# Performance work log

Measured on AMD Instinct MI355X. Metric: run time of the kernel, lower is better.

The kernel has to match this reference:

```python
import jax, jax.numpy as jnp
import numpy as np

NUM_HEADS = 8
ATTN_DIM = 512
DIM_HEAD = ATTN_DIM // NUM_HEADS
SCALE = DIM_HEAD ** -0.5
GN_EPS = 1e-5


def setup_inputs() -> dict:
    key = jax.random.key(0)
    k1, k2, k3 = jax.random.split(key, 3)
    B, H, W, C_IN, C_OUT = 8, 32, 32, 256, 256
    x = jax.random.normal(k1, (B, H, W, C_IN), dtype=jnp.float32)
    w_qkv = jax.random.normal(k2, (C_IN, 3 * ATTN_DIM), dtype=jnp.float32) * (C_IN ** -0.5)
    w_out = jax.random.normal(k3, (ATTN_DIM, C_OUT), dtype=jnp.float32) * (ATTN_DIM ** -0.5)
    b_out = jnp.zeros((C_OUT,), dtype=jnp.float32)
    gamma = jnp.ones((C_OUT,), dtype=jnp.float32)
    beta = jnp.zeros((C_OUT,), dtype=jnp.float32)
    return {"x": x, "w_qkv": w_qkv, "w_out": w_out, "b_out": b_out, "gamma": gamma, "beta": beta}


def reference(x, w_qkv, w_out, b_out, gamma, beta):
    B, H, W, _ = x.shape
    N = H * W
    # 1x1 conv QKV projection (no bias)
    qkv = jnp.einsum('bhwc,cd->bhwd', x, w_qkv)
    q, k, v = jnp.split(qkv, 3, axis=-1)
    # NHWC -> (B, heads, dim_head, HW), matching tf transpose+reshape
    def to_heads(t):
        return t.transpose(0, 3, 1, 2).reshape(B, NUM_HEADS, DIM_HEAD, N)
    q = to_heads(q) * SCALE
    k = to_heads(k)
    v = to_heads(v)
    # sim = q^T k over dim_head: (B, heads, N_q, N_k)
    sim = jnp.einsum('bhcn,bhcm->bhnm', q, k)
    attn = jax.nn.softmax(sim, axis=-1)  # includes the max-subtraction of the original
    # out = attn @ v^T: (B, heads, N, dim_head)
    out = jnp.einsum('bhnm,bhcm->bhnc', attn, v)
    # faithful tf.reshape((B,-1,H,W)) then NCHW->NHWC transpose
    out = out.reshape(B, -1, H, W).transpose(0, 2, 3, 1)  # (B, H, W, attn_dim)
    # output 1x1 conv (with bias) + GroupNorm(groups=1): normalize over (H, W, C) per sample
    y = jnp.einsum('bhwc,cd->bhwd', out, w_out) + b_out
    mean = jnp.mean(y, axis=(1, 2, 3), keepdims=True)
    var = jnp.var(y, axis=(1, 2, 3), keepdims=True)
    y = (y - mean) * jax.lax.rsqrt(var + GN_EPS)
    return y * gamma + beta
```

## Files before the change

### kernel.cpp

```cpp
#include <hip/hip_runtime.h>
#include <math.h>

#define NPOS   1024
#define CIN    256
#define DQKV   1536
#define ATTND  512
#define HEADS  8
#define DH     64
#define COUT   256
#define NBATCH 8
#define SCALE  0.125f
#define GN_EPS 1e-5f

typedef __attribute__((ext_vector_type(8))) __bf16 bf16x8;
typedef __attribute__((ext_vector_type(4))) __bf16 bf16x4;
typedef __attribute__((ext_vector_type(4))) float floatx4;
typedef __attribute__((ext_vector_type(8))) unsigned short ushort8;

#if __has_builtin(__builtin_amdgcn_exp2f)
#define EXP2(x) __builtin_amdgcn_exp2f(x)
#else
#define EXP2(x) exp2f(x)
#endif

#define GLOAD16(G, L) __builtin_amdgcn_global_load_lds( \
    (const __attribute__((address_space(1))) void*)(G), \
    (__attribute__((address_space(3))) void*)(L), 16, 0, 0)

#define OFF_XB   (0ull)
#define OFF_WT   (4ull*1048576)
#define OFF_WOT  (4ull*1048576 + 786432ull)
#define OFF_QB   (5ull*1048576)
#define OFF_KB   (13ull*1048576)
#define OFF_VT   (29ull*1048576)
#define OFF_O2TT (45ull*1048576)
#define OFF_ST   (53ull*1048576)

__device__ inline ushort8 cvt_bf8(float4 a, float4 b) {
    bf16x8 o;
    o[0] = (__bf16)a.x; o[1] = (__bf16)a.y; o[2] = (__bf16)a.z; o[3] = (__bf16)a.w;
    o[4] = (__bf16)b.x; o[5] = (__bf16)b.y; o[6] = (__bf16)b.z; o[7] = (__bf16)b.w;
    return *(ushort8*)&o;
}

__global__ __launch_bounds__(256) void prep(
    const float* __restrict__ x,
    const float* __restrict__ w_qkv, const float* __restrict__ w_out,
    unsigned short* __restrict__ xb,
    unsigned short* __restrict__ wT, unsigned short* __restrict__ woT,
    float* __restrict__ stats)
{
    const int bid = blockIdx.x;
    const int t = threadIdx.x;
    __shared__ unsigned short tile[64][68];

    if (bid == 0) stats[t] = 0.0f;

    if (bid >= 128) {
        const size_t base = (size_t)(bid - 128) * 8192 + (size_t)t * 8;
        #pragma unroll
        for (int i = 0; i < 4; ++i) {
            const size_t off = base + (size_t)i * 2048;
            const float4 u = *(const float4*)&x[off];
            const float4 v = *(const float4*)&x[off + 4];
            *(ushort8*)&xb[off] = cvt_bf8(u, v);
        }
        return;
    }

    if (bid < 96) {
        const int n0 = (bid >> 2) * 64, k0 = (bid & 3) * 64;
        #pragma unroll
        for (int p = 0; p < 4; ++p) {
            const int row = p * 16 + (t >> 4);
            const int c = (t & 15) * 4;
            float4 a = *(const float4*)&w_qkv[(size_t)(k0 + row) * DQKV + n0 + c];
            float sv[4] = {a.x, a.y, a.z, a.w};
            #pragma unroll
            for (int j = 0; j < 4; ++j) {
                const float sc = (n0 + c + j) < 512 ? (SCALE * 1.44269504088896f) : 1.0f;
                __bf16 hb = (__bf16)(sv[j] * sc);
                tile[row][c + j] = *(unsigned short*)&hb;
            }
        }
        __syncthreads();
        const int nn = t >> 2;
        const int kc = (t & 3) * 16;
        unsigned short tmp[16];
        #pragma unroll
        for (int j = 0; j < 16; ++j) tmp[j] = tile[kc + j][nn];
        *(ushort8*)&wT[(size_t)(n0 + nn) * 256 + k0 + kc]     = *(ushort8*)&tmp[0];
        *(ushort8*)&wT[(size_t)(n0 + nn) * 256 + k0 + kc + 8] = *(ushort8*)&tmp[8];
        return;
    }

    const int idx = bid - 96;
    const int d0 = (idx & 3) * 64, k0 = (idx >> 2) * 64;
    #pragma unroll
    for (int p = 0; p < 4; ++p) {
        const int row = p * 16 + (t >> 4);
        const int c = (t & 15) * 4;
        float4 a = *(const float4*)&w_out[(size_t)(k0 + row) * COUT + d0 + c];
        float sv[4] = {a.x, a.y, a.z, a.w};
        #pragma unroll
        for (int j = 0; j < 4; ++j) {
            __bf16 hb = (__bf16)sv[j];
            tile[row][c + j] = *(unsigned short*)&hb;
        }
    }
    __syncthreads();
    {
        const int nn = t >> 2;
        const int kc = (t & 3) * 16;
        unsigned short tmp[16];
        #pragma unroll
        for (int j = 0; j < 16; ++j) tmp[j] = tile[kc + j][nn];
        *(ushort8*)&woT[(size_t)(d0 + nn) * 512 + k0 + kc]     = *(ushort8*)&tmp[0];
        *(ushort8*)&woT[(size_t)(d0 + nn) * 512 + k0 + kc + 8] = *(ushort8*)&tmp[8];
    }
}

__global__ __launch_bounds__(256) void qkv_gemm_mfma(
    const unsigned short* __restrict__ xb, const __bf16* __restrict__ wT,
    __bf16* __restrict__ qb, __bf16* __restrict__ kb, __bf16* __restrict__ vT)
{
    const int bid = blockIdx.x;
    const int xcd = bid & 7, local = bid >> 3;
    const int m0 = (xcd * 8 + (local & 7)) * 128;
    const int n0 = (local >> 3) * 128;

    const int t = threadIdx.x;
    const int w = t >> 6, lane = t & 63;
    const int col = lane & 15, qd = lane >> 4;
    const int wm = w >> 1, wn = w & 1;

    __shared__ __align__(16) unsigned short As[2][128][32];
    __shared__ __align__(16) unsigned short Bs[2][128][32];

    floatx4 zero4 = {0.f, 0.f, 0.f, 0.f};
    floatx4 acc[4][4];
    #pragma unroll
    for (int i = 0; i < 4; ++i)
        #pragma unroll
        for (int j = 0; j < 4; ++j) acc[i][j] = zero4;

    const int arow = lane >> 2;
    const int soff = (((lane & 3) ^ ((lane >> 3) & 3)) << 4);
    const char* xsrc = (const char*)xb + (size_t)(m0 + w * 16 + arow) * 512 + soff;
    const char* wsrc = (const char*)wT + (size_t)(n0 + w * 16 + arow) * 512 + soff;

#define QSTAGE(B, KK) do {                                            \
    GLOAD16(xsrc + (KK) * 64,             &As[B][w * 16][0]);         \
    GLOAD16(xsrc + 32768 + (KK) * 64,     &As[B][64 + w * 16][0]);    \
    GLOAD16(wsrc + (KK) * 64,             &Bs[B][w * 16][0]);         \
    GLOAD16(wsrc + 32768 + (KK) * 64,     &Bs[B][64 + w * 16][0]);    \
} while (0)

    QSTAGE(0, 0);
    __syncthreads();

    const int rsw = ((col >> 1) & 3);
    const int fro = ((qd ^ rsw) << 4);

    int cur = 0;
    for (int kk = 0; kk < 8; ++kk) {
        if (kk < 7) QSTAGE(cur ^ 1, kk + 1);

        bf16x8 wf[4];
        #pragma unroll
        for (int ct = 0; ct < 4; ++ct)
            wf[ct] = *(const bf16x8*)((const char*)&Bs[cur][wn * 64 + ct * 16 + col][0] + fro);
        #pragma unroll
        for (int st = 0; st < 4; ++st) {
            bf16x8 xf = *(const bf16x8*)((const char*)&As[cur][wm * 64 + st * 16 + col][0] + fro);
            #pragma unroll
            for (int ct = 0; ct < 4; ++ct)
                acc[ct][st] = __builtin_amdgcn_mfma_f32_16x16x32_bf16(wf[ct], xf, acc[ct][st], 0, 0, 0);
        }
        __syncthreads();
        cur ^= 1;
    }
#undef QSTAGE

    #pragma unroll
    for (int ct = 0; ct < 4; ++ct) {
        const int cbase = n0 + wn * 64 + ct * 16;
        const int sect = cbase >> 9;
        const int hh = (cbase >> 6) & 7;
        const int dd = (cbase & 63) + qd * 4;
        if (sect < 2) {
            __bf16* base = (sect == 0) ? qb : kb;
            #pragma unroll
            for (int st = 0; st < 4; ++st) {
                const int m = m0 + wm * 64 + st * 16 + col;
                const int b_ = m >> 10, n = m & 1023;
                bf16x4 o;
                #pragma unroll
                for (int r = 0; r < 4; ++r) o[r] = (__bf16)acc[ct][st][r];
                *(bf16x4*)&base[(((size_t)b_ * HEADS + hh) * NPOS + n) * DH + dd] = o;
            }
        } else {
            #pragma unroll
            for (int st = 0; st < 4; ++st) {
                const int m = m0 + wm * 64 + st * 16 + col;
                const int b_ = m >> 10, n = m & 1023;
                const size_t rowbase = ((size_t)(b_ * HEADS + hh) * DH + dd) * NPOS + n;
                #pragma unroll
                for (int r = 0; r < 4; ++r)
                    vT[rowbase + (size_t)r * NPOS] = (__bf16)acc[ct][st][r];
            }
        }
    }
}

__global__ __launch_bounds__(256, 2) void attn_mfma(
    const __bf16* __restrict__ qg, const __bf16* __restrict__ kg,
    const __bf16* __restrict__ vTg, __bf16* __restrict__ o2tT)
{
    const int bid = blockIdx.x;
    const int rid = (bid & 7) * 64 + (bid >> 3);
    const int qblk = rid & 7, h = (rid >> 3) & 7, b = rid >> 6;
    const int bh = b * HEADS + h;
    const int t = threadIdx.x;
    const int w = t >> 6, lane = t & 63;
    const int col = lane & 15;
    const int qd = lane >> 4;

    __shared__ __align__(16) unsigned short Kbuf[2][64][64];
    __shared__ __align__(16) unsigned short Vbuf[2][64][64];
    __shared__ __align__(16) unsigned short ps[4][32][68];

    bf16x8 qf0[2], qf1[2];
    #pragma unroll
    for (int s = 0; s < 2; ++s) {
        const __bf16* qptr = qg + ((size_t)bh * NPOS + qblk * 128 + s * 64 + w * 16 + col) * DH;
        qf0[s] = *(const bf16x8*)(qptr + qd * 8);
        qf1[s] = *(const bf16x8*)(qptr + 32 + qd * 8);
    }

    const char* kByte = (const char*)kg  + (size_t)bh * NPOS * DH * 2;
    const char* vByte = (const char*)vTg + (size_t)bh * DH * NPOS * 2;
    const int rsub = lane >> 3;
    const int csw  = ((lane & 7) * 16) ^ (rsub << 4);
    const char* ksrc0 = kByte + (size_t)(w * 8 + rsub) * 128  + csw;
    const char* vsrc0 = vByte + (size_t)(w * 8 + rsub) * 2048 + csw;

#define STAGE(B, KT) do {                                                    \
    const char* ks_ = ksrc0 + (size_t)(KT) * 8192;                           \
    const char* vs_ = vsrc0 + (size_t)(KT) * 128;                            \
    GLOAD16(ks_,         &Kbuf[B][0][0] + w * 512);                          \
    GLOAD16(ks_ + 4096,  &Kbuf[B][0][0] + 2048 + w * 512);                   \
    GLOAD16(vs_,         &Vbuf[B][0][0] + w * 512);                          \
    GLOAD16(vs_ + 65536, &Vbuf[B][0][0] + 2048 + w * 512);                   \
} while (0)

    floatx4 zero4 = {0.f, 0.f, 0.f, 0.f};
    floatx4 accO[2][4];
    #pragma unroll
    for (int s = 0; s < 2; ++s)
        #pragma unroll
        for (int i = 0; i < 4; ++i) accO[s][i] = zero4;
    floatx4 accL[2] = {zero4, zero4};
    bf16x8 ones8;
    #pragma unroll
    for (int j = 0; j < 8; ++j) ones8[j] = (__bf16)1.0f;

    const int swzc = (col & 7) << 4;
    const int offF0 = (qd * 16) ^ swzc;
    const int offF1 = (64 + qd * 16) ^ swzc;

    STAGE(0, 0);
    __syncthreads();

    int cur = 0;
    for (int kt = 0; kt < 16; ++kt) {
        if (kt < 15) STAGE(cur ^ 1, kt + 1);

        floatx4 accS[2][4];
        #pragma unroll
        for (int mt = 0; mt < 4; ++mt) {
            const char* krow = (const char*)&Kbuf[cur][mt * 16 + col][0];
            bf16x8 kf0 = *(const bf16x8*)(krow + offF0);
            bf16x8 kf1 = *(const bf16x8*)(krow + offF1);
            #pragma unroll
            for (int s = 0; s < 2; ++s) {
                accS[s][mt] = __builtin_amdgcn_mfma_f32_16x16x32_bf16(kf0, qf0[s], zero4, 0, 0, 0);
                accS[s][mt] = __builtin_amdgcn_mfma_f32_16x16x32_bf16(kf1, qf1[s], accS[s][mt], 0, 0, 0);
            }
        }

        #pragma unroll
        for (int s = 0; s < 2; ++s)
            #pragma unroll
            for (int mt = 0; mt < 4; ++mt) {
                bf16x4 pv;
                #pragma unroll
                for (int r = 0; r < 4; ++r) pv[r] = (__bf16)EXP2(accS[s][mt][r]);
                *(bf16x4*)&ps[w][s * 16 + col][mt * 16 + qd * 4] = pv;
            }

        bf16x8 pf0[2], pf1[2];
        #pragma unroll
        for (int s = 0; s < 2; ++s) {
            pf0[s] = *(const bf16x8*)&ps[w][s * 16 + col][qd * 8];
            pf1[s] = *(const bf16x8*)&ps[w][s * 16 + col][32 + qd * 8];
            accL[s] = __builtin_amdgcn_mfma_f32_16x16x32_bf16(ones8, pf0[s], accL[s], 0, 0, 0);
            accL[s] = __builtin_amdgcn_mfma_f32_16x16x32_bf16(ones8, pf1[s], accL[s], 0, 0, 0);
        }

        #pragma unroll
        for (int ct = 0; ct < 4; ++ct) {
            const char* vrow = (const char*)&Vbuf[cur][ct * 16 + col][0];
            bf16x8 vf0 = *(const bf16x8*)(vrow + offF0);
            bf16x8 vf1 = *(const bf16x8*)(vrow + offF1);
            #pragma unroll
            for (int s = 0; s < 2; ++s) {
                accO[s][ct] = __builtin_amdgcn_mfma_f32_16x16x32_bf16(vf0, pf0[s], accO[s][ct], 0, 0, 0);
                accO[s][ct] = __builtin_amdgcn_mfma_f32_16x16x32_bf16(vf1, pf1[s], accO[s][ct], 0, 0, 0);
            }
        }
        __syncthreads();
        cur ^= 1;
    }
#undef STAGE

    float inv_l[2];
    #pragma unroll
    for (int s = 0; s < 2; ++s) inv_l[s] = 1.0f / accL[s][0];

    unsigned short (*obuf)[8][68] = (unsigned short (*)[8][68])ps;
    __syncthreads();
    #pragma unroll
    for (int s = 0; s < 2; ++s)
        #pragma unroll
        for (int ct = 0; ct < 4; ++ct) {
            bf16x4 o;
            #pragma unroll
            for (int r = 0; r < 4; ++r) o[r] = (__bf16)(accO[s][ct][r] * inv_l[s]);
            *(bf16x4*)&obuf[col][s * 4 + w][ct * 16 + qd * 4] = o;
        }
    __syncthreads();
    const int chbase = h * 64 + qblk * 8;
    #pragma unroll
    for (int i = 0; i < 4; ++i) {
        const int p = i * 256 + t;
        const int pc = p >> 6, cc = p & 63;
        bf16x8 o;
        #pragma unroll
        for (int j = 0; j < 8; ++j) {
            unsigned short u = obuf[pc][j][cc];
            o[j] = *(__bf16*)&u;
        }
        *(bf16x8*)&o2tT[((size_t)b * NPOS + p) * ATTND + chbase] = o;
    }
}

__global__ __launch_bounds__(256) void out_mfma(
    const __bf16* __restrict__ a, const __bf16* __restrict__ woT,
    const float* __restrict__ b_out, float* __restrict__ y,
    float* __restrict__ stats)
{
    const int bid = blockIdx.x;
    const int xcd = bid & 7, local = bid >> 3;
    const int m0 = (xcd * 16 + (local & 15)) * 64;
    const int d0 = (local >> 4) * 64;
    const int b = xcd;

    const int t = threadIdx.x;
    const int w = t >> 6, lane = t & 63;
    const int col = lane & 15, qd = lane >> 4;
    const int wm = w >> 1, wn = w & 1;

    __shared__ __align__(16) unsigned short As[64][72];
    __shared__ __align__(16) unsigned short Bs[64][72];
    __shared__ float reds[4], redq[4];

    floatx4 zero4 = {0.f, 0.f, 0.f, 0.f};
    floatx4 acc[2][2];
    #pragma unroll
    for (int i = 0; i < 2; ++i)
        #pragma unroll
        for (int j = 0; j < 2; ++j) acc[i][j] = zero4;

    const int lrow = t >> 2, lc = (t & 3) * 16;

    for (int k0 = 0; k0 < ATTND; k0 += 64) {
        __syncthreads();
        *(ushort8*)&As[lrow][lc]     = *(const ushort8*)&a[(size_t)(m0 + lrow) * ATTND + k0 + lc];
        *(ushort8*)&As[lrow][lc + 8] = *(const ushort8*)&a[(size_t)(m0 + lrow) * ATTND + k0 + lc + 8];
        *(ushort8*)&Bs[lrow][lc]     = *(const ushort8*)&woT[(size_t)(d0 + lrow) * ATTND + k0 + lc];
        *(ushort8*)&Bs[lrow][lc + 8] = *(const ushort8*)&woT[(size_t)(d0 + lrow) * ATTND + k0 + lc + 8];
        __syncthreads();
        bf16x8 af0[2], af1[2];
        #pragma unroll
        for (int mt = 0; mt < 2; ++mt) {
            af0[mt] = *(const bf16x8*)&As[wm * 32 + mt * 16 + col][qd * 8];
            af1[mt] = *(const bf16x8*)&As[wm * 32 + mt * 16 + col][32 + qd * 8];
        }
        #pragma unroll
        for (int nt = 0; nt < 2; ++nt) {
            bf16x8 bf0 = *(const bf16x8*)&Bs[wn * 32 + nt * 16 + col][qd * 8];
            bf16x8 bf1 = *(const bf16x8*)&Bs[wn * 32 + nt * 16 + col][32 + qd * 8];
            #pragma unroll
            for (int mt = 0; mt < 2; ++mt) {
                acc[mt][nt] = __builtin_amdgcn_mfma_f32_16x16x32_bf16(af0[mt], bf0, acc[mt][nt], 0, 0, 0);
                acc[mt][nt] = __builtin_amdgcn_mfma_f32_16x16x32_bf16(af1[mt], bf1, acc[mt][nt], 0, 0, 0);
            }
        }
    }

    float bias_n[2];
    #pragma unroll
    for (int nt = 0; nt < 2; ++nt) bias_n[nt] = b_out[d0 + wn * 32 + nt * 16 + col];

    float bsum = 0.0f, bsq = 0.0f;
    #pragma unroll
    for (int mt = 0; mt < 2; ++mt) {
        #pragma unroll
        for (int r = 0; r < 4; ++r) {
            const int m = m0 + wm * 32 + mt * 16 + qd * 4 + r;
            const int p = m & 1023;
            #pragma unroll
            for (int nt = 0; nt < 2; ++nt) {
                const int d = d0 + wn * 32 + nt * 16 + col;
                const float v = acc[mt][nt][r] + bias_n[nt];
                y[((size_t)b * NPOS + p) * COUT + d] = v;
                bsum += v;
                bsq  += v * v;
            }
        }
    }
    #pragma unroll
    for (int off = 1; off < 64; off <<= 1) {
        bsum += __shfl_xor(bsum, off);
        bsq  += __shfl_xor(bsq, off);
    }
    if (lane == 0) { reds[w] = bsum; redq[w] = bsq; }
    __syncthreads();
    if (t == 0) {
        atomicAdd(&stats[b * 16],       reds[0] + reds[1] + reds[2] + reds[3]);
        atomicAdd(&stats[128 + b * 16], redq[0] + redq[1] + redq[2] + redq[3]);
    }
}

__global__ __launch_bounds__(256) void gn_finalize(
    float* __restrict__ y, const float* __restrict__ stats,
    const float* __restrict__ gamma, const float* __restrict__ beta)
{
    const int idx = blockIdx.x * 256 + threadIdx.x;
    const int e = idx * 4;
    const int b_ = e >> 18;
    const int d = e & (COUT - 1);
    const float invn = 1.0f / (float)(NPOS * COUT);
    const float mean = stats[b_ * 16] * invn;
    const float var  = stats[128 + b_ * 16] * invn - mean * mean;
    const float rsig = rsqrtf(var + GN_EPS);
    float4 vv = *(float4*)&y[e];
    const float4 g  = *(const float4*)&gamma[d];
    const float4 bt = *(const float4*)&beta[d];
    vv.x = (vv.x - mean) * rsig * g.x + bt.x;
    vv.y = (vv.y - mean) * rsig * g.y + bt.y;
    vv.z = (vv.z - mean) * rsig * g.z + bt.z;
    vv.w = (vv.w - mean) * rsig * g.w + bt.w;
    *(float4*)&y[e] = vv;
}

extern "C" void kernel_launch(void* const* d_in, const int* in_sizes, int n_in,
                              void* d_out, int out_size, void* d_ws, size_t ws_size,
                              hipStream_t stream)
{
    const float* x     = (const float*)d_in[0];
    const float* w_qkv = (const float*)d_in[1];
    const float* w_out = (const float*)d_in[2];
    const float* b_out = (const float*)d_in[3];
    const float* gamma = (const float*)d_in[4];
    const float* beta  = (const float*)d_in[5];
    float* out = (float*)d_out;
    char* ws = (char*)d_ws;

    unsigned short* xb  = (unsigned short*)(ws + OFF_XB);
    unsigned short* wT  = (unsigned short*)(ws + OFF_WT);
    unsigned short* woT = (unsigned short*)(ws + OFF_WOT);
    __bf16* qb  = (__bf16*)(ws + OFF_QB);
    __bf16* kb  = (__bf16*)(ws + OFF_KB);
    __bf16* vT  = (__bf16*)(ws + OFF_VT);
    __bf16* o2tT = (__bf16*)(ws + OFF_O2TT);
    float* stats = (float*)(ws + OFF_ST);

    prep         <<<dim3(384),  256, 0, stream>>>(x, w_qkv, w_out, xb, wT, woT, stats);
    qkv_gemm_mfma<<<dim3(768),  256, 0, stream>>>(xb, (const __bf16*)wT, qb, kb, vT);
    attn_mfma    <<<dim3(512),  256, 0, stream>>>(qb, kb, vT, o2tT);
    out_mfma     <<<dim3(512),  256, 0, stream>>>(o2tT, (const __bf16*)woT, b_out, out, stats);
    gn_finalize  <<<dim3(2048), 256, 0, stream>>>(out, stats, gamma, beta);
}
```

Before: 124.6 us.

## Fuse all five stages into one cooperative persistent kernel with grid syncs

Merges the prep, QKV GEMM, attention, output GEMM and GroupNorm finalize kernels into a single cooperative kernel of 512 blocks that separates the stages with grid.sync(). The aim is to remove four kernel launch boundaries and the gaps between them. The QKV GEMM's 768 tiles become a grid-stride loop, and all stages share one shared-memory buffer. The cost is a fixed grid size, occupancy limited to two blocks per CU, and grid-wide barrier overhead, with the old multi-kernel path kept as a fallback if the cooperative launch fails.

```diff
diff --git a/kernel.cpp b/kernel.cpp
--- a/kernel.cpp
+++ b/kernel.cpp
@@ -1,5 +1,8 @@
 #include <hip/hip_runtime.h>
+#include <hip/hip_cooperative_groups.h>
 #include <math.h>
+
+namespace cg = cooperative_groups;
 
 #define NPOS   1024
 #define CIN    256
@@ -41,6 +44,414 @@
     o[0] = (__bf16)a.x; o[1] = (__bf16)a.y; o[2] = (__bf16)a.z; o[3] = (__bf16)a.w;
     o[4] = (__bf16)b.x; o[5] = (__bf16)b.y; o[6] = (__bf16)b.z; o[7] = (__bf16)b.w;
     return *(ushort8*)&o;
+}
+
+__global__ __launch_bounds__(256, 2) void mega(
+    const float* __restrict__ x, const float* __restrict__ w_qkv,
+    const float* __restrict__ w_out, const float* __restrict__ b_out,
+    const float* __restrict__ gamma, const float* __restrict__ beta,
+    float* __restrict__ y,
+    unsigned short* __restrict__ xb, unsigned short* __restrict__ wT,
+    unsigned short* __restrict__ woT,
+    __bf16* __restrict__ qb, __bf16* __restrict__ kb, __bf16* __restrict__ vT,
+    __bf16* __restrict__ o2tT, float* __restrict__ stats)
+{
+    cg::grid_group grid = cg::this_grid();
+    const int bid = blockIdx.x;
+    const int t = threadIdx.x;
+    __shared__ __align__(16) unsigned char SM[50176];
+
+    if (bid < 384) {
+        unsigned short (*tile)[68] = (unsigned short (*)[68])SM;
+        if (bid == 0) stats[t] = 0.0f;
+        if (bid >= 128) {
+            const size_t base = (size_t)(bid - 128) * 8192 + (size_t)t * 8;
+            #pragma unroll
+            for (int i = 0; i < 4; ++i) {
+                const size_t off = base + (size_t)i * 2048;
+                const float4 u = *(const float4*)&x[off];
+                const float4 v = *(const float4*)&x[off + 4];
+                *(ushort8*)&xb[off] = cvt_bf8(u, v);
+            }
+        } else if (bid < 96) {
+            const int n0 = (bid >> 2) * 64, k0 = (bid & 3) * 64;
+            #pragma unroll
+            for (int p = 0; p < 4; ++p) {
+                const int row = p * 16 + (t >> 4);
+                const int c = (t & 15) * 4;
+                float4 a = *(const float4*)&w_qkv[(size_t)(k0 + row) * DQKV + n0 + c];
+                float sv[4] = {a.x, a.y, a.z, a.w};
+                #pragma unroll
+                for (int j = 0; j < 4; ++j) {
+                    const float sc = (n0 + c + j) < 512 ? (SCALE * 1.44269504088896f) : 1.0f;
+                    __bf16 hb = (__bf16)(sv[j] * sc);
+                    tile[row][c + j] = *(unsigned short*)&hb;
+                }
+            }
+            __syncthreads();
+            const int nn = t >> 2;
+            const int kc = (t & 3) * 16;
+            unsigned short tmp[16];
+            #pragma unroll
+            for (int j = 0; j < 16; ++j) tmp[j] = tile[kc + j][nn];
+            *(ushort8*)&wT[(size_t)(n0 + nn) * 256 + k0 + kc]     = *(ushort8*)&tmp[0];
+            *(ushort8*)&wT[(size_t)(n0 + nn) * 256 + k0 + kc + 8] = *(ushort8*)&tmp[8];
+        } else {
+            const int idx = bid - 96;
+            const int d0 = (idx & 3) * 64, k0 = (idx >> 2) * 64;
+            #pragma unroll
+            for (int p = 0; p < 4; ++p) {
+                const int row = p * 16 + (t >> 4);
+                const int c = (t & 15) * 4;
+                float4 a = *(const float4*)&w_out[(size_t)(k0 + row) * COUT + d0 + c];
+                float sv[4] = {a.x, a.y, a.z, a.w};
+                #pragma unroll
+                for (int j = 0; j < 4; ++j) {
+                    __bf16 hb = (__bf16)sv[j];
+                    tile[row][c + j] = *(unsigned short*)&hb;
+                }
+            }
+            __syncthreads();
+            const int nn = t >> 2;
+            const int kc = (t & 3) * 16;
+            unsigned short tmp[16];
+            #pragma unroll
+            for (int j = 0; j < 16; ++j) tmp[j] = tile[kc + j][nn];
+            *(ushort8*)&woT[(size_t)(d0 + nn) * 512 + k0 + kc]     = *(ushort8*)&tmp[0];
+            *(ushort8*)&woT[(size_t)(d0 + nn) * 512 + k0 + kc + 8] = *(ushort8*)&tmp[8];
+        }
+    }
+    grid.sync();
+
+    {
+        unsigned short (*As)[128][32] = (unsigned short (*)[128][32])SM;
+        unsigned short (*Bs)[128][32] = (unsigned short (*)[128][32])(SM + 16384);
+        const int w = t >> 6, lane = t & 63;
+        const int col = lane & 15, qd = lane >> 4;
+        const int wm = w >> 1, wn = w & 1;
+        const int arow = lane >> 2;
+        const int soff = (((lane & 3) ^ ((lane >> 3) & 3)) << 4);
+        const int rsw = ((col >> 1) & 3);
+        const int fro = ((qd ^ rsw) << 4);
+        floatx4 zero4 = {0.f, 0.f, 0.f, 0.f};
+
+#define QSTAGE(B, KK) do {                                            \
+    GLOAD16(xsrc + (KK) * 64,             &As[B][w * 16][0]);         \
+    GLOAD16(xsrc + 32768 + (KK) * 64,     &As[B][64 + w * 16][0]);    \
+    GLOAD16(wsrc + (KK) * 64,             &Bs[B][w * 16][0]);         \
+    GLOAD16(wsrc + 32768 + (KK) * 64,     &Bs[B][64 + w * 16][0]);    \
+} while (0)
+
+        for (int tid = bid; tid < 768; tid += 512) {
+            const int xcd = tid & 7, local = tid >> 3;
+            const int m0 = (xcd * 8 + (local & 7)) * 128;
+            const int n0 = (local >> 3) * 128;
+
+            floatx4 acc[4][4];
+            #pragma unroll
+            for (int i = 0; i < 4; ++i)
+                #pragma unroll
+                for (int j = 0; j < 4; ++j) acc[i][j] = zero4;
+
+            const char* xsrc = (const char*)xb + (size_t)(m0 + w * 16 + arow) * 512 + soff;
+            const char* wsrc = (const char*)wT + (size_t)(n0 + w * 16 + arow) * 512 + soff;
+
+            __syncthreads();
+            QSTAGE(0, 0);
+            __syncthreads();
+
+            int cur = 0;
+            for (int kk = 0; kk < 8; ++kk) {
+                if (kk < 7) QSTAGE(cur ^ 1, kk + 1);
+                bf16x8 wf[4];
+                #pragma unroll
+                for (int ct = 0; ct < 4; ++ct)
+                    wf[ct] = *(const bf16x8*)((const char*)&Bs[cur][wn * 64 + ct * 16 + col][0] + fro);
+                #pragma unroll
+                for (int st = 0; st < 4; ++st) {
+                    bf16x8 xf = *(const bf16x8*)((const char*)&As[cur][wm * 64 + st * 16 + col][0] + fro);
+                    #pragma unroll
+                    for (int ct = 0; ct < 4; ++ct)
+                        acc[ct][st] = __builtin_amdgcn_mfma_f32_16x16x32_bf16(wf[ct], xf, acc[ct][st], 0, 0, 0);
+                }
+                __syncthreads();
+                cur ^= 1;
+            }
+
+            #pragma unroll
+            for (int ct = 0; ct < 4; ++ct) {
+                const int cbase = n0 + wn * 64 + ct * 16;
+                const int sect = cbase >> 9;
+                const int hh = (cbase >> 6) & 7;
+                const int dd = (cbase & 63) + qd * 4;
+                if (sect < 2) {
+                    __bf16* base = (sect == 0) ? qb : kb;
+                    #pragma unroll
+                    for (int st = 0; st < 4; ++st) {
+                        const int m = m0 + wm * 64 + st * 16 + col;
+                        const int b_ = m >> 10, n = m & 1023;
+                        bf16x4 o;
+                        #pragma unroll
+                        for (int r = 0; r < 4; ++r) o[r] = (__bf16)acc[ct][st][r];
+                        *(bf16x4*)&base[(((size_t)b_ * HEADS + hh) * NPOS + n) * DH + dd] = o;
+                    }
+                } else {
+                    #pragma unroll
+                    for (int st = 0; st < 4; ++st) {
+                        const int m = m0 + wm * 64 + st * 16 + col;
+                        const int b_ = m >> 10, n = m & 1023;
+                        const size_t rowbase = ((size_t)(b_ * HEADS + hh) * DH + dd) * NPOS + n;
+                        #pragma unroll
+                        for (int r = 0; r < 4; ++r)
+                            vT[rowbase + (size_t)r * NPOS] = (__bf16)acc[ct][st][r];
+                    }
+                }
+            }
+        }
+#undef QSTAGE
+    }
+    grid.sync();
+
+    {
+        unsigned short (*Kbuf)[64][64] = (unsigned short (*)[64][64])SM;
+        unsigned short (*Vbuf)[64][64] = (unsigned short (*)[64][64])(SM + 16384);
+        unsigned short (*ps)[32][68]   = (unsigned short (*)[32][68])(SM + 32768);
+
+        const int rid = (bid & 7) * 64 + (bid >> 3);
+        const int qblk = rid & 7, h = (rid >> 3) & 7, b = rid >> 6;
+        const int bh = b * HEADS + h;
+        const int w = t >> 6, lane = t & 63;
+        const int col = lane & 15;
+        const int qd = lane >> 4;
+
+        bf16x8 qf0[2], qf1[2];
+        #pragma unroll
+        for (int s = 0; s < 2; ++s) {
+            const __bf16* qptr = qb + ((size_t)bh * NPOS + qblk * 128 + s * 64 + w * 16 + col) * DH;
+            qf0[s] = *(const bf16x8*)(qptr + qd * 8);
+            qf1[s] = *(const bf16x8*)(qptr + 32 + qd * 8);
+        }
+
+        const char* kByte = (const char*)kb + (size_t)bh * NPOS * DH * 2;
+        const char* vByte = (const char*)vT + (size_t)bh * DH * NPOS * 2;
+        const int rsub = lane >> 3;
+        const int csw  = ((lane & 7) * 16) ^ (rsub << 4);
+        const char* ksrc0 = kByte + (size_t)(w * 8 + rsub) * 128  + csw;
+        const char* vsrc0 = vByte + (size_t)(w * 8 + rsub) * 2048 + csw;
+
+#define STAGE(B, KT) do {                                                    \
+    const char* ks_ = ksrc0 + (size_t)(KT) * 8192;                           \
+    const char* vs_ = vsrc0 + (size_t)(KT) * 128;                            \
+    GLOAD16(ks_,         &Kbuf[B][0][0] + w * 512);                          \
+    GLOAD16(ks_ + 4096,  &Kbuf[B][0][0] + 2048 + w * 512);                   \
+    GLOAD16(vs_,         &Vbuf[B][0][0] + w * 512);                          \
+    GLOAD16(vs_ + 65536, &Vbuf[B][0][0] + 2048 + w * 512);                   \
+} while (0)
+
+        floatx4 zero4 = {0.f, 0.f, 0.f, 0.f};
+        floatx4 accO[2][4];
+        #pragma unroll
+        for (int s = 0; s < 2; ++s)
+            #pragma unroll
+            for (int i = 0; i < 4; ++i) accO[s][i] = zero4;
+        floatx4 accL[2] = {zero4, zero4};
+        bf16x8 ones8;
+        #pragma unroll
+        for (int j = 0; j < 8; ++j) ones8[j] = (__bf16)1.0f;
+
+        const int swzc = (col & 7) << 4;
+        const int offF0 = (qd * 16) ^ swzc;
+        const int offF1 = (64 + qd * 16) ^ swzc;
+
+        STAGE(0, 0);
+        __syncthreads();
+
+        int cur = 0;
+        for (int kt = 0; kt < 16; ++kt) {
+            if (kt < 15) STAGE(cur ^ 1, kt + 1);
+
+            floatx4 accS[2][4];
+            #pragma unroll
+            for (int mt = 0; mt < 4; ++mt) {
+                const char* krow = (const char*)&Kbuf[cur][mt * 16 + col][0];
+                bf16x8 kf0 = *(const bf16x8*)(krow + offF0);
+                bf16x8 kf1 = *(const bf16x8*)(krow + offF1);
+                #pragma unroll
+                for (int s = 0; s < 2; ++s) {
+                    accS[s][mt] = __builtin_amdgcn_mfma_f32_16x16x32_bf16(kf0, qf0[s], zero4, 0, 0, 0);
+                    accS[s][mt] = __builtin_amdgcn_mfma_f32_16x16x32_bf16(kf1, qf1[s], accS[s][mt], 0, 0, 0);
+                }
+            }
+
+            #pragma unroll
+            for (int s = 0; s < 2; ++s)
+                #pragma unroll
+                for (int mt = 0; mt < 4; ++mt) {
+                    bf16x4 pv;
+                    #pragma unroll
+                    for (int r = 0; r < 4; ++r) pv[r] = (__bf16)EXP2(accS[s][mt][r]);
+                    *(bf16x4*)&ps[w][s * 16 + col][mt * 16 + qd * 4] = pv;
+                }
+
+            bf16x8 pf0[2], pf1[2];
+            #pragma unroll
+            for (int s = 0; s < 2; ++s) {
+                pf0[s] = *(const bf16x8*)&ps[w][s * 16 + col][qd * 8];
+                pf1[s] = *(const bf16x8*)&ps[w][s * 16 + col][32 + qd * 8];
+                accL[s] = __builtin_amdgcn_mfma_f32_16x16x32_bf16(ones8, pf0[s], accL[s], 0, 0, 0);
+                accL[s] = __builtin_amdgcn_mfma_f32_16x16x32_bf16(ones8, pf1[s], accL[s], 0, 0, 0);
+            }
+
+            #pragma unroll
+            for (int ct = 0; ct < 4; ++ct) {
+                const char* vrow = (const char*)&Vbuf[cur][ct * 16 + col][0];
+                bf16x8 vf0 = *(const bf16x8*)(vrow + offF0);
+                bf16x8 vf1 = *(const bf16x8*)(vrow + offF1);
+                #pragma unroll
+                for (int s = 0; s < 2; ++s) {
+                    accO[s][ct] = __builtin_amdgcn_mfma_f32_16x16x32_bf16(vf0, pf0[s], accO[s][ct], 0, 0, 0);
+                    accO[s][ct] = __builtin_amdgcn_mfma_f32_16x16x32_bf16(vf1, pf1[s], accO[s][ct], 0, 0, 0);
+                }
+            }
+            __syncthreads();
+            cur ^= 1;
+        }
+#undef STAGE
+
+        float inv_l[2];
+        #pragma unroll
+        for (int s = 0; s < 2; ++s) inv_l[s] = 1.0f / accL[s][0];
+
+        unsigned short (*obuf)[8][68] = (unsigned short (*)[8][68])ps;
+        __syncthreads();
+        #pragma unroll
+        for (int s = 0; s < 2; ++s)
+            #pragma unroll
+            for (int ct = 0; ct < 4; ++ct) {
+                bf16x4 o;
+                #pragma unroll
+                for (int r = 0; r < 4; ++r) o[r] = (__bf16)(accO[s][ct][r] * inv_l[s]);
+                *(bf16x4*)&obuf[col][s * 4 + w][ct * 16 + qd * 4] = o;
+            }
+        __syncthreads();
+        const int chbase = h * 64 + qblk * 8;
+        #pragma unroll
+        for (int i = 0; i < 4; ++i) {
+            const int p = i * 256 + t;
+            const int pc = p >> 6, cc = p & 63;
+            bf16x8 o;
+            #pragma unroll
+            for (int j = 0; j < 8; ++j) {
+                unsigned short u = obuf[pc][j][cc];
+                o[j] = *(__bf16*)&u;
+            }
+            *(bf16x8*)&o2tT[((size_t)b * NPOS + p) * ATTND + chbase] = o;
+        }
+    }
+    grid.sync();
+
+    {
+        unsigned short (*oAs)[72] = (unsigned short (*)[72])SM;
+        unsigned short (*oBs)[72] = (unsigned short (*)[72])(SM + 16384);
+        float* reds = (float*)(SM + 32768);
+        float* redq = reds + 4;
+
+        const int xcd = bid & 7, local = bid >> 3;
+        const int m0 = (xcd * 16 + (local & 15)) * 64;
+        const int d0 = (local >> 4) * 64;
+        const int b = xcd;
+
+        const int w = t >> 6, lane = t & 63;
+        const int col = lane & 15, qd = lane >> 4;
+        const int wm = w >> 1, wn = w & 1;
+
+        floatx4 zero4 = {0.f, 0.f, 0.f, 0.f};
+        floatx4 acc[2][2];
+        #pragma unroll
+        for (int i = 0; i < 2; ++i)
+            #pragma unroll
+            for (int j = 0; j < 2; ++j) acc[i][j] = zero4;
+
+        const int lrow = t >> 2, lc = (t & 3) * 16;
+
+        for (int k0 = 0; k0 < ATTND; k0 += 64) {
+            __syncthreads();
+            *(ushort8*)&oAs[lrow][lc]     = *(const ushort8*)&o2tT[(size_t)(m0 + lrow) * ATTND + k0 + lc];
+            *(ushort8*)&oAs[lrow][lc + 8] = *(const ushort8*)&o2tT[(size_t)(m0 + lrow) * ATTND + k0 + lc + 8];
+            *(ushort8*)&oBs[lrow][lc]     = *(const ushort8*)&((const __bf16*)woT)[(size_t)(d0 + lrow) * ATTND + k0 + lc];
+            *(ushort8*)&oBs[lrow][lc + 8] = *(const ushort8*)&((const __bf16*)woT)[(size_t)(d0 + lrow) * ATTND + k0 + lc + 8];
+            __syncthreads();
+            bf16x8 af0[2], af1[2];
+            #pragma unroll
+            for (int mt = 0; mt < 2; ++mt) {
+                af0[mt] = *(const bf16x8*)&oAs[wm * 32 + mt * 16 + col][qd * 8];
+                af1[mt] = *(const bf16x8*)&oAs[wm * 32 + mt * 16 + col][32 + qd * 8];
+            }
+            #pragma unroll
+            for (int nt = 0; nt < 2; ++nt) {
+                bf16x8 bf0 = *(const bf16x8*)&oBs[wn * 32 + nt * 16 + col][qd * 8];
+                bf16x8 bf1 = *(const bf16x8*)&oBs[wn * 32 + nt * 16 + col][32 + qd * 8];
+                #pragma unroll
+                for (int mt = 0; mt < 2; ++mt) {
+                    acc[mt][nt] = __builtin_amdgcn_mfma_f32_16x16x32_bf16(af0[mt], bf0, acc[mt][nt], 0, 0, 0);
+                    acc[mt][nt] = __builtin_amdgcn_mfma_f32_16x16x32_bf16(af1[mt], bf1, acc[mt][nt], 0, 0, 0);
+                }
+            }
+        }
+
+        float bias_n[2];
+        #pragma unroll
+        for (int nt = 0; nt < 2; ++nt) bias_n[nt] = b_out[d0 + wn * 32 + nt * 16 + col];
+
+        float bsum = 0.0f, bsq = 0.0f;
+        #pragma unroll
+        for (int mt = 0; mt < 2; ++mt) {
+            #pragma unroll
+            for (int r = 0; r < 4; ++r) {
+                const int m = m0 + wm * 32 + mt * 16 + qd * 4 + r;
+                const int p = m & 1023;
+                #pragma unroll
+                for (int nt = 0; nt < 2; ++nt) {
+                    const int d = d0 + wn * 32 + nt * 16 + col;
+                    const float v = acc[mt][nt][r] + bias_n[nt];
+                    y[((size_t)b * NPOS + p) * COUT + d] = v;
+                    bsum += v;
+                    bsq  += v * v;
+                }
+            }
+        }
+        #pragma unroll
+        for (int off = 1; off < 64; off <<= 1) {
+            bsum += __shfl_xor(bsum, off);
+            bsq  += __shfl_xor(bsq, off);
+        }
+        if (lane == 0) { reds[w] = bsum; redq[w] = bsq; }
+        __syncthreads();
+        if (t == 0) {
+            atomicAdd(&stats[b * 16],       reds[0] + reds[1] + reds[2] + reds[3]);
+            atomicAdd(&stats[128 + b * 16], redq[0] + redq[1] + redq[2] + redq[3]);
+        }
+    }
+    grid.sync();
+
+    for (int i = bid; i < 2048; i += 512) {
+        const int idx = i * 256 + t;
+        const int e = idx * 4;
+        const int b_ = e >> 18;
+        const int d = e & (COUT - 1);
+        const float invn = 1.0f / (float)(NPOS * COUT);
+        const float mean = stats[b_ * 16] * invn;
+        const float var  = stats[128 + b_ * 16] * invn - mean * mean;
+        const float rsig = rsqrtf(var + GN_EPS);
+        float4 vv = *(float4*)&y[e];
+        const float4 g  = *(const float4*)&gamma[d];
+        const float4 bt = *(const float4*)&beta[d];
+        vv.x = (vv.x - mean) * rsig * g.x + bt.x;
+        vv.y = (vv.y - mean) * rsig * g.y + bt.y;
+        vv.z = (vv.z - mean) * rsig * g.z + bt.z;
+        vv.w = (vv.w - mean) * rsig * g.w + bt.w;
+        *(float4*)&y[e] = vv;
+    }
 }
 
 __global__ __launch_bounds__(256) void prep(
@@ -487,9 +898,20 @@
     __bf16* o2tT = (__bf16*)(ws + OFF_O2TT);
     float* stats = (float*)(ws + OFF_ST);
 
-    prep         <<<dim3(384),  256, 0, stream>>>(x, w_qkv, w_out, xb, wT, woT, stats);
-    qkv_gemm_mfma<<<dim3(768),  256, 0, stream>>>(xb, (const __bf16*)wT, qb, kb, vT);
-    attn_mfma    <<<dim3(512),  256, 0, stream>>>(qb, kb, vT, o2tT);
-    out_mfma     <<<dim3(512),  256, 0, stream>>>(o2tT, (const __bf16*)woT, b_out, out, stats);
-    gn_finalize  <<<dim3(2048), 256, 0, stream>>>(out, stats, gamma, beta);
+    void* kargs[] = {
+        (void*)&x, (void*)&w_qkv, (void*)&w_out, (void*)&b_out,
+        (void*)&gamma, (void*)&beta, (void*)&out,
+        (void*)&xb, (void*)&wT, (void*)&woT,
+        (void*)&qb, (void*)&kb, (void*)&vT, (void*)&o2tT, (void*)&stats
+    };
+    hipError_t err = hipLaunchCooperativeKernel(
+        (const void*)mega, dim3(512), dim3(256), kargs, 0, stream);
+
+    if (err != hipSuccess) {
+        prep         <<<dim3(384),  256, 0, stream>>>(x, w_qkv, w_out, xb, wT, woT, stats);
+        qkv_gemm_mfma<<<dim3(768),  256, 0, stream>>>(xb, (const __bf16*)wT, qb, kb, vT);
+        attn_mfma    <<<dim3(512),  256, 0, stream>>>(qb, kb, vT, o2tT);
+        out_mfma     <<<dim3(512),  256, 0, stream>>>(o2tT, (const __bf16*)woT, b_out, out, stats);
+        gn_finalize  <<<dim3(2048), 256, 0, stream>>>(out, stats, gamma, beta);
+    }
 }
```

After: 409.9 us. 3.29x slower.
